# Optimization experiments

Measured on AMD Instinct MI355X. Metric: run time of the kernel, lower is better.

## Reference

```python
import jax, jax.numpy as jnp
import numpy as np

B, N, D, C, H = 8, 128, 128, 32, 256  # jets, tracks, track feat, context feat, net hidden


def _pair_idx(n):
    # row-major off-diagonal indices == order of torch boolean indexing x[adjmat]
    m = ~np.eye(n, dtype=bool)
    i, j = np.nonzero(m)
    return jnp.asarray(i), jnp.asarray(j)  # each (n*(n-1),)


def setup_inputs() -> dict:
    key = jax.random.key(0)
    ks = jax.random.split(key, 8)
    x = jax.random.normal(ks[0], (B, N, D), jnp.float32)
    context = jax.random.normal(ks[1], (B, C), jnp.float32)
    in_dim = 2 * D + C
    W1 = jax.random.normal(ks[2], (in_dim, H), jnp.float32) / np.float32(np.sqrt(in_dim))
    b1 = jnp.zeros((H,), jnp.float32)
    W2 = jax.random.normal(ks[3], (H, 1), jnp.float32) / np.float32(np.sqrt(H))
    b2 = jnp.zeros((1,), jnp.float32)
    # vertex labels: -1 denotes 'unique' (no vertex), excluded from matches
    labels = jax.random.randint(ks[4], (B, N), -1, 10, jnp.int64)
    origin = jax.random.randint(ks[5], (B, N), 0, 7, jnp.int64)
    return {"x": x, "context": context, "W1": W1, "b1": b1, "W2": W2, "b2": b2,
            "labels": labels, "origin": origin}


def reference(x, context, W1, b1, W2, b2, labels, origin):
    b, n, d = x.shape
    c = context.shape[-1]
    i_idx, j_idx = _pair_idx(n)           # static off-diagonal pair pattern (masks=None)
    P = i_idx.shape[0]                    # n*(n-1) pairs per jet

    # packed pair features: tt[:, :d] = x[b,i], tt[:, d:] = x[b,j]
    left = x[:, i_idx]                    # (b, P, d)
    right = x[:, j_idx]                   # (b, P, d)
    tt = jnp.concatenate([left, right], axis=-1).reshape(b * P, 2 * d)
    # context is the same per-jet row for every pair
    ctx = jnp.broadcast_to(context[:, None, :], (b, P, c)).reshape(b * P, c)

    # Dense net with context concat: (E, 2d+c) -> relu(H) -> 1 logit
    h = jax.nn.relu(jnp.concatenate([tt, ctx], axis=-1) @ W1 + b1)
    pred = h @ W2 + b2                    # (E, 1)

    # ---- loss (BCEWithLogits, pair weights, normalized by #matches) ----
    li, lj = labels[:, i_idx], labels[:, j_idx]
    match = ((li == lj) & (li >= 0) & (lj >= 0)).reshape(-1).astype(pred.dtype)  # (E,)
    z = pred[:, 0]
    bce = jnp.maximum(z, 0) - z * match + jnp.log1p(jnp.exp(-jnp.abs(z)))

    o = origin.astype(jnp.int32)
    w = jnp.clip((o == 3).astype(jnp.int32) + (o == 4).astype(jnp.int32)
                 + (o == 5).astype(jnp.int32), 0, 1) - (o == 1).astype(jnp.int32)
    pw = (w[:, i_idx] & w[:, j_idx]).reshape(-1)          # bitwise AND as in torch
    weights = (1 + pw).astype(pred.dtype)

    task_weight = jnp.asarray(1.0, pred.dtype)
    loss = (bce * weights).sum() / match.sum() * task_weight
    return pred, loss
```

## Files before the change

kernel.cpp:

```cpp
#include <hip/hip_runtime.h>
#include <math.h>

#define BB 8
#define NN 128
#define DD 128
#define CC 32
#define HH 256
#define PP 16256
#define ROWS (BB*NN)
#define NBUCK 64
#define TI 32
#define TJ 16
#define LPAD 260


__global__ __launch_bounds__(256) void k1_stage(
    const float* __restrict__ x, const float* __restrict__ ctx,
    const float* __restrict__ W1, const float* __restrict__ b1,
    float* __restrict__ Lp, float* __restrict__ Rp,
    float* __restrict__ buckets)
{
    __shared__ float xs[4 * DD];
    __shared__ float cs[CC];
    const int t  = threadIdx.x;
    const int r0 = blockIdx.x * 4;
    const int b  = r0 >> 7;

    if (blockIdx.x == 0 && t < 2 * NBUCK + 1) buckets[t] = 0.f;

    if (t < 128) ((float4*)xs)[t] = ((const float4*)(x + r0 * DD))[t];
    else if (t < 128 + CC) cs[t - 128] = ctx[b * CC + (t - 128)];
    __syncthreads();

    const int h = t;
    float accL[4] = {0.f, 0.f, 0.f, 0.f};
    float accR[4] = {0.f, 0.f, 0.f, 0.f};

#pragma unroll 8
    for (int k = 0; k < DD; ++k) {
        const float wl = W1[k * HH + h];
        const float wr = W1[(k + DD) * HH + h];
#pragma unroll
        for (int r = 0; r < 4; ++r) {
            const float xv = xs[r * DD + k];
            accL[r] = fmaf(xv, wl, accL[r]);
            accR[r] = fmaf(xv, wr, accR[r]);
        }
    }

    float cb = b1[h];
#pragma unroll 4
    for (int c = 0; c < CC; ++c) cb = fmaf(cs[c], W1[(2 * DD + c) * HH + h], cb);

#pragma unroll
    for (int r = 0; r < 4; ++r) {
        Lp[(r0 + r) * HH + h] = accL[r] + cb;
        Rp[(r0 + r) * HH + h] = accR[r];
    }
}

__global__ __launch_bounds__(256) void k2_pairs(
    const float* __restrict__ Lp, const float* __restrict__ Rp,
    const float* __restrict__ W2, const float* __restrict__ b2,
    const int* __restrict__ labels, const int* __restrict__ origin,
    float* __restrict__ pred, float* __restrict__ buckets,
    int* __restrict__ counter, float* __restrict__ loss)
{
    __shared__ float Ls[TI][LPAD];
    __shared__ float Rs[TJ][LPAD];
    __shared__ float sred[8];
    __shared__ int amLast;

    const int tid = threadIdx.x;
    const int blk = blockIdx.x;
    const int b   = blk >> 5;
    const int i0  = ((blk >> 3) & 3) * TI;
    const int j0  = (blk & 7) * TJ;

#pragma unroll
    for (int q = 0; q < 8; ++q) {
        const int idx = q * 256 + tid;
        const int r   = idx >> 6;
        const int c4  = (idx & 63) * 4;
        *(float4*)(&Ls[r][c4]) = *(const float4*)(Lp + (b * NN + i0 + r) * HH + c4);
    }
#pragma unroll
    for (int q = 0; q < 4; ++q) {
        const int idx = q * 256 + tid;
        const int r   = idx >> 6;
        const int c4  = (idx & 63) * 4;
        *(float4*)(&Rs[r][c4]) = *(const float4*)(Rp + (b * NN + j0 + r) * HH + c4);
    }
    __syncthreads();

    const int ti = tid >> 4, tj = tid & 15;
    float4 acc0 = make_float4(0.f, 0.f, 0.f, 0.f);
    float4 acc1 = make_float4(0.f, 0.f, 0.f, 0.f);
#pragma unroll 8
    for (int hc = 0; hc < HH / 4; ++hc) {
        const float4 l0 = *(const float4*)(&Ls[ti][hc * 4]);
        const float4 l1 = *(const float4*)(&Ls[ti + 16][hc * 4]);
        const float4 r  = *(const float4*)(&Rs[tj][hc * 4]);
        const float4 w  = ((const float4*)W2)[hc];
        acc0.x = fmaf(fmaxf(l0.x + r.x, 0.f), w.x, acc0.x);
        acc0.y = fmaf(fmaxf(l0.y + r.y, 0.f), w.y, acc0.y);
        acc0.z = fmaf(fmaxf(l0.z + r.z, 0.f), w.z, acc0.z);
        acc0.w = fmaf(fmaxf(l0.w + r.w, 0.f), w.w, acc0.w);
        acc1.x = fmaf(fmaxf(l1.x + r.x, 0.f), w.x, acc1.x);
        acc1.y = fmaf(fmaxf(l1.y + r.y, 0.f), w.y, acc1.y);
        acc1.z = fmaf(fmaxf(l1.z + r.z, 0.f), w.z, acc1.z);
        acc1.w = fmaf(fmaxf(l1.w + r.w, 0.f), w.w, acc1.w);
    }

    const int i  = i0 + ti;
    const int i2 = i + 16;
    const int j  = j0 + tj;
    const float b2v = b2[0];
    const float z0 = acc0.x + acc0.y + acc0.z + acc0.w + b2v;
    const float z1 = acc1.x + acc1.y + acc1.z + acc1.w + b2v;

    float bcew = 0.f, mt = 0.f;
    const int lj = labels[b * NN + j];
    const int oj = origin[b * NN + j];
    const int wj = (oj == 3 || oj == 4 || oj == 5) ? 1 : ((oj == 1) ? -1 : 0);
    if (i != j) {
        pred[b * PP + i * 127 + j - (j > i ? 1 : 0)] = z0;
        const int li = labels[b * NN + i];
        const float match = (li == lj && li >= 0) ? 1.f : 0.f;
        const int oi = origin[b * NN + i];
        const int wi = (oi == 3 || oi == 4 || oi == 5) ? 1 : ((oi == 1) ? -1 : 0);
        const float weight = (float)(1 + (wi & wj));
        bcew += (fmaxf(z0, 0.f) - z0 * match + log1pf(expf(-fabsf(z0)))) * weight;
        mt += match;
    }
    if (i2 != j) {
        pred[b * PP + i2 * 127 + j - (j > i2 ? 1 : 0)] = z1;
        const int li = labels[b * NN + i2];
        const float match = (li == lj && li >= 0) ? 1.f : 0.f;
        const int oi = origin[b * NN + i2];
        const int wi = (oi == 3 || oi == 4 || oi == 5) ? 1 : ((oi == 1) ? -1 : 0);
        const float weight = (float)(1 + (wi & wj));
        bcew += (fmaxf(z1, 0.f) - z1 * match + log1pf(expf(-fabsf(z1)))) * weight;
        mt += match;
    }

#pragma unroll
    for (int m = 1; m < 64; m <<= 1) {
        bcew += __shfl_xor(bcew, m, 64);
        mt   += __shfl_xor(mt, m, 64);
    }
    const int w64 = tid >> 6, lane = tid & 63;
    if (lane == 0) { sred[w64] = bcew; sred[4 + w64] = mt; }
    __syncthreads();
    if (tid == 0) {
        const float s1 = sred[0] + sred[1] + sred[2] + sred[3];
        const float s2 = sred[4] + sred[5] + sred[6] + sred[7];
        const int bkt = blk & (NBUCK - 1);
        atomicAdd(buckets + bkt, s1);
        atomicAdd(buckets + NBUCK + bkt, s2);
        __threadfence();
        const int old = atomicAdd(counter, 1);
        amLast = (old == (int)gridDim.x - 1) ? 1 : 0;
    }
    __syncthreads();

    if (amLast && tid < 64) {
        float v1 = atomicAdd(buckets + tid, 0.f);
        float v2 = atomicAdd(buckets + NBUCK + tid, 0.f);
#pragma unroll
        for (int m = 1; m < 64; m <<= 1) {
            v1 += __shfl_xor(v1, m, 64);
            v2 += __shfl_xor(v2, m, 64);
        }
        if (tid == 0) loss[0] = v1 / v2;
    }
}

extern "C" void kernel_launch(void* const* d_in, const int* in_sizes, int n_in,
                              void* d_out, int out_size, void* d_ws, size_t ws_size,
                              hipStream_t stream)
{
    const float* x      = (const float*)d_in[0];
    const float* ctx    = (const float*)d_in[1];
    const float* W1     = (const float*)d_in[2];
    const float* b1     = (const float*)d_in[3];
    const float* W2     = (const float*)d_in[4];
    const float* b2     = (const float*)d_in[5];
    const int*   labels = (const int*)d_in[6];
    const int*   origin = (const int*)d_in[7];

    float* pred = (float*)d_out;
    float* loss = pred + BB * PP;

    float* Lp      = (float*)d_ws;
    float* Rp      = Lp + ROWS * HH;
    float* buckets = Rp + ROWS * HH;
    int*   counter = (int*)(buckets + 2 * NBUCK);

    k1_stage<<<ROWS / 4, 256, 0, stream>>>(x, ctx, W1, b1, Lp, Rp, buckets);
    k2_pairs<<<256, 256, 0, stream>>>(Lp, Rp, W2, b2, labels, origin,
                                      pred, buckets, counter, loss);
}
```

Baseline: 97.33 us.

## Retile stage and pair kernels for more register reuse per thread

The stage kernel now gives each block 16 rows and a 64-wide slice of the hidden dimension, with 4 row-groups per block. This lets each W1 column load be shared across more rows and cuts the grid from 256 to 256 differently shaped blocks. The pair kernel drops to 128 threads, each computing a 2x2 block of pairs instead of 2x1, so every LDS read of L and R feeds more FMAs. The cost is half as many waves per pair block, which means less latency hiding, and more registers per thread.

```diff
diff --git a/kernel.cpp b/kernel.cpp
--- a/kernel.cpp
+++ b/kernel.cpp
@@ -20,19 +20,27 @@
     float* __restrict__ Lp, float* __restrict__ Rp,
     float* __restrict__ buckets)
 {
-    __shared__ float xs[4 * DD];
+    __shared__ float xs[16 * DD];
     __shared__ float cs[CC];
-    const int t  = threadIdx.x;
-    const int r0 = blockIdx.x * 4;
-    const int b  = r0 >> 7;
-
-    if (blockIdx.x == 0 && t < 2 * NBUCK + 1) buckets[t] = 0.f;
-
-    if (t < 128) ((float4*)xs)[t] = ((const float4*)(x + r0 * DD))[t];
-    else if (t < 128 + CC) cs[t - 128] = ctx[b * CC + (t - 128)];
-    __syncthreads();
-
-    const int h = t;
+    const int t   = threadIdx.x;
+    const int blk = blockIdx.x;
+    const int rg  = blk >> 2;
+    const int hq  = blk & 3;
+    const int r0  = rg * 16;
+    const int b   = r0 >> 7;
+    const int h0  = hq * 64;
+
+    if (blk == 0 && t < 2 * NBUCK + 1) buckets[t] = 0.f;
+
+    ((float4*)xs)[t]       = ((const float4*)(x + r0 * DD))[t];
+    ((float4*)xs)[t + 256] = ((const float4*)(x + r0 * DD))[t + 256];
+    if (t < CC) cs[t] = ctx[b * CC + t];
+    __syncthreads();
+
+    const int hl = t & 63;
+    const int rq = t >> 6;
+    const int h  = h0 + hl;
+
     float accL[4] = {0.f, 0.f, 0.f, 0.f};
     float accR[4] = {0.f, 0.f, 0.f, 0.f};
 
@@ -42,7 +50,7 @@
         const float wr = W1[(k + DD) * HH + h];
 #pragma unroll
         for (int r = 0; r < 4; ++r) {
-            const float xv = xs[r * DD + k];
+            const float xv = xs[(rq * 4 + r) * DD + k];
             accL[r] = fmaf(xv, wl, accL[r]);
             accR[r] = fmaf(xv, wr, accR[r]);
         }
@@ -54,12 +62,12 @@
 
 #pragma unroll
     for (int r = 0; r < 4; ++r) {
-        Lp[(r0 + r) * HH + h] = accL[r] + cb;
-        Rp[(r0 + r) * HH + h] = accR[r];
+        Lp[(r0 + rq * 4 + r) * HH + h] = accL[r] + cb;
+        Rp[(r0 + rq * 4 + r) * HH + h] = accR[r];
     }
 }
 
-__global__ __launch_bounds__(256) void k2_pairs(
+__global__ __launch_bounds__(128) void k2_pairs(
     const float* __restrict__ Lp, const float* __restrict__ Rp,
     const float* __restrict__ W2, const float* __restrict__ b2,
     const int* __restrict__ labels, const int* __restrict__ origin,
@@ -68,7 +76,7 @@
 {
     __shared__ float Ls[TI][LPAD];
     __shared__ float Rs[TJ][LPAD];
-    __shared__ float sred[8];
+    __shared__ float sred[4];
     __shared__ int amLast;
 
     const int tid = threadIdx.x;
@@ -78,70 +86,86 @@
     const int j0  = (blk & 7) * TJ;
 
 #pragma unroll
-    for (int q = 0; q < 8; ++q) {
-        const int idx = q * 256 + tid;
+    for (int q = 0; q < 16; ++q) {
+        const int idx = q * 128 + tid;
         const int r   = idx >> 6;
         const int c4  = (idx & 63) * 4;
         *(float4*)(&Ls[r][c4]) = *(const float4*)(Lp + (b * NN + i0 + r) * HH + c4);
     }
 #pragma unroll
-    for (int q = 0; q < 4; ++q) {
-        const int idx = q * 256 + tid;
+    for (int q = 0; q < 8; ++q) {
+        const int idx = q * 128 + tid;
         const int r   = idx >> 6;
         const int c4  = (idx & 63) * 4;
         *(float4*)(&Rs[r][c4]) = *(const float4*)(Rp + (b * NN + j0 + r) * HH + c4);
     }
     __syncthreads();
 
-    const int ti = tid >> 4, tj = tid & 15;
-    float4 acc0 = make_float4(0.f, 0.f, 0.f, 0.f);
-    float4 acc1 = make_float4(0.f, 0.f, 0.f, 0.f);
+    const int ti = tid >> 3, tj = tid & 7;
+    float4 a00 = make_float4(0.f, 0.f, 0.f, 0.f);
+    float4 a01 = make_float4(0.f, 0.f, 0.f, 0.f);
+    float4 a10 = make_float4(0.f, 0.f, 0.f, 0.f);
+    float4 a11 = make_float4(0.f, 0.f, 0.f, 0.f);
 #pragma unroll 8
     for (int hc = 0; hc < HH / 4; ++hc) {
         const float4 l0 = *(const float4*)(&Ls[ti][hc * 4]);
         const float4 l1 = *(const float4*)(&Ls[ti + 16][hc * 4]);
-        const float4 r  = *(const float4*)(&Rs[tj][hc * 4]);
+        const float4 r0 = *(const float4*)(&Rs[tj][hc * 4]);
+        const float4 r1 = *(const float4*)(&Rs[tj + 8][hc * 4]);
         const float4 w  = ((const float4*)W2)[hc];
-        acc0.x = fmaf(fmaxf(l0.x + r.x, 0.f), w.x, acc0.x);
-        acc0.y = fmaf(fmaxf(l0.y + r.y, 0.f), w.y, acc0.y);
-        acc0.z = fmaf(fmaxf(l0.z + r.z, 0.f), w.z, acc0.z);
-        acc0.w = fmaf(fmaxf(l0.w + r.w, 0.f), w.w, acc0.w);
-        acc1.x = fmaf(fmaxf(l1.x + r.x, 0.f), w.x, acc1.x);
-        acc1.y = fmaf(fmaxf(l1.y + r.y, 0.f), w.y, acc1.y);
-        acc1.z = fmaf(fmaxf(l1.z + r.z, 0.f), w.z, acc1.z);
-        acc1.w = fmaf(fmaxf(l1.w + r.w, 0.f), w.w, acc1.w);
-    }
-
-    const int i  = i0 + ti;
-    const int i2 = i + 16;
-    const int j  = j0 + tj;
+        a00.x = fmaf(fmaxf(l0.x + r0.x, 0.f), w.x, a00.x);
+        a00.y = fmaf(fmaxf(l0.y + r0.y, 0.f), w.y, a00.y);
+        a00.z = fmaf(fmaxf(l0.z + r0.z, 0.f), w.z, a00.z);
+        a00.w = fmaf(fmaxf(l0.w + r0.w, 0.f), w.w, a00.w);
+        a01.x = fmaf(fmaxf(l0.x + r1.x, 0.f), w.x, a01.x);
+        a01.y = fmaf(fmaxf(l0.y + r1.y, 0.f), w.y, a01.y);
+        a01.z = fmaf(fmaxf(l0.z + r1.z, 0.f), w.z, a01.z);
+        a01.w = fmaf(fmaxf(l0.w + r1.w, 0.f), w.w, a01.w);
+        a10.x = fmaf(fmaxf(l1.x + r0.x, 0.f), w.x, a10.x);
+        a10.y = fmaf(fmaxf(l1.y + r0.y, 0.f), w.y, a10.y);
+        a10.z = fmaf(fmaxf(l1.z + r0.z, 0.f), w.z, a10.z);
+        a10.w = fmaf(fmaxf(l1.w + r0.w, 0.f), w.w, a10.w);
+        a11.x = fmaf(fmaxf(l1.x + r1.x, 0.f), w.x, a11.x);
+        a11.y = fmaf(fmaxf(l1.y + r1.y, 0.f), w.y, a11.y);
+        a11.z = fmaf(fmaxf(l1.z + r1.z, 0.f), w.z, a11.z);
+        a11.w = fmaf(fmaxf(l1.w + r1.w, 0.f), w.w, a11.w);
+    }
+
+    const int ia[2] = { i0 + ti, i0 + ti + 16 };
+    const int ja[2] = { j0 + tj, j0 + tj + 8 };
     const float b2v = b2[0];
-    const float z0 = acc0.x + acc0.y + acc0.z + acc0.w + b2v;
-    const float z1 = acc1.x + acc1.y + acc1.z + acc1.w + b2v;
+    float z[2][2];
+    z[0][0] = a00.x + a00.y + a00.z + a00.w + b2v;
+    z[0][1] = a01.x + a01.y + a01.z + a01.w + b2v;
+    z[1][0] = a10.x + a10.y + a10.z + a10.w + b2v;
+    z[1][1] = a11.x + a11.y + a11.z + a11.w + b2v;
+
+    int li[2], wi[2], lj[2], wj[2];
+#pragma unroll
+    for (int u = 0; u < 2; ++u) {
+        li[u] = labels[b * NN + ia[u]];
+        lj[u] = labels[b * NN + ja[u]];
+        const int oi = origin[b * NN + ia[u]];
+        const int oj = origin[b * NN + ja[u]];
+        wi[u] = (oi == 3 || oi == 4 || oi == 5) ? 1 : ((oi == 1) ? -1 : 0);
+        wj[u] = (oj == 3 || oj == 4 || oj == 5) ? 1 : ((oj == 1) ? -1 : 0);
+    }
 
     float bcew = 0.f, mt = 0.f;
-    const int lj = labels[b * NN + j];
-    const int oj = origin[b * NN + j];
-    const int wj = (oj == 3 || oj == 4 || oj == 5) ? 1 : ((oj == 1) ? -1 : 0);
-    if (i != j) {
-        pred[b * PP + i * 127 + j - (j > i ? 1 : 0)] = z0;
-        const int li = labels[b * NN + i];
-        const float match = (li == lj && li >= 0) ? 1.f : 0.f;
-        const int oi = origin[b * NN + i];
-        const int wi = (oi == 3 || oi == 4 || oi == 5) ? 1 : ((oi == 1) ? -1 : 0);
-        const float weight = (float)(1 + (wi & wj));
-        bcew += (fmaxf(z0, 0.f) - z0 * match + log1pf(expf(-fabsf(z0)))) * weight;
-        mt += match;
-    }
-    if (i2 != j) {
-        pred[b * PP + i2 * 127 + j - (j > i2 ? 1 : 0)] = z1;
-        const int li = labels[b * NN + i2];
-        const float match = (li == lj && li >= 0) ? 1.f : 0.f;
-        const int oi = origin[b * NN + i2];
-        const int wi = (oi == 3 || oi == 4 || oi == 5) ? 1 : ((oi == 1) ? -1 : 0);
-        const float weight = (float)(1 + (wi & wj));
-        bcew += (fmaxf(z1, 0.f) - z1 * match + log1pf(expf(-fabsf(z1)))) * weight;
-        mt += match;
+#pragma unroll
+    for (int u = 0; u < 2; ++u) {
+#pragma unroll
+        for (int v = 0; v < 2; ++v) {
+            const int i = ia[u], j = ja[v];
+            if (i != j) {
+                const float zz = z[u][v];
+                pred[b * PP + i * 127 + j - (j > i ? 1 : 0)] = zz;
+                const float match = (li[u] == lj[v] && li[u] >= 0) ? 1.f : 0.f;
+                const float weight = (float)(1 + (wi[u] & wj[v]));
+                bcew += (fmaxf(zz, 0.f) - zz * match + log1pf(expf(-fabsf(zz)))) * weight;
+                mt += match;
+            }
+        }
     }
 
 #pragma unroll
@@ -150,11 +174,11 @@
         mt   += __shfl_xor(mt, m, 64);
     }
     const int w64 = tid >> 6, lane = tid & 63;
-    if (lane == 0) { sred[w64] = bcew; sred[4 + w64] = mt; }
+    if (lane == 0) { sred[w64] = bcew; sred[2 + w64] = mt; }
     __syncthreads();
     if (tid == 0) {
-        const float s1 = sred[0] + sred[1] + sred[2] + sred[3];
-        const float s2 = sred[4] + sred[5] + sred[6] + sred[7];
+        const float s1 = sred[0] + sred[1];
+        const float s2 = sred[2] + sred[3];
         const int bkt = blk & (NBUCK - 1);
         atomicAdd(buckets + bkt, s1);
         atomicAdd(buckets + NBUCK + bkt, s2);
@@ -197,7 +221,7 @@
     float* buckets = Rp + ROWS * HH;
     int*   counter = (int*)(buckets + 2 * NBUCK);
 
-    k1_stage<<<ROWS / 4, 256, 0, stream>>>(x, ctx, W1, b1, Lp, Rp, buckets);
-    k2_pairs<<<256, 256, 0, stream>>>(Lp, Rp, W2, b2, labels, origin,
+    k1_stage<<<256, 256, 0, stream>>>(x, ctx, W1, b1, Lp, Rp, buckets);
+    k2_pairs<<<256, 128, 0, stream>>>(Lp, Rp, W2, b2, labels, origin,
                                       pred, buckets, counter, loss);
 }
```

Result: slower. 100.5 us (+3.2%).
